# Optimization experiments

Measured on AMD Instinct MI355X. Metric: run time of the kernel, lower is better.

The kernel has to match this reference:

```python
import jax, jax.numpy as jnp
import numpy as np

DIM = 2048
N_HEADS = 16
HEAD_DIM = DIM // N_HEADS

def setup_inputs() -> dict:
    key = jax.random.key(0)
    kx, kqkv, kout = jax.random.split(key, 3)
    x = jax.random.normal(kx, (2, 2048, DIM), dtype=jnp.float32)
    # nn.Linear weights stored [out_features, in_features]; y = x @ W.T
    W_qkv = jax.random.normal(kqkv, (3 * DIM, DIM), dtype=jnp.float32) * (DIM ** -0.5)
    W_out = jax.random.normal(kout, (DIM, DIM), dtype=jnp.float32) * (DIM ** -0.5)
    return {"x": x, "W_qkv": W_qkv, "W_out": W_out}

def reference(x, W_qkv, W_out):
    B, T, D = x.shape
    qkv = jnp.einsum('btd,ed->bte', x, W_qkv)  # [B,T,3D]
    q, k, v = jnp.split(qkv, 3, axis=-1)
    def heads(t):
        return t.reshape(B, T, N_HEADS, HEAD_DIM).transpose(0, 2, 1, 3)  # [B,H,T,d]
    q, k, v = heads(q), heads(k), heads(v)
    att = jnp.einsum('bhid,bhjd->bhij', q, k) / (HEAD_DIM ** 0.5)
    causal = jnp.tril(jnp.ones((T, T), dtype=bool))
    att = jnp.where(causal, att, -jnp.inf)
    att = jax.nn.softmax(att, axis=-1)
    out = jnp.einsum('bhij,bhjd->bhid', att, v)
    out = out.transpose(0, 2, 1, 3).reshape(B, T, D)
    return jnp.einsum('btd,ed->bte', out, W_out)
```

## Files before the change

### kernel.cpp

```cpp
#include <hip/hip_runtime.h>

typedef short short8 __attribute__((ext_vector_type(8)));
typedef short short4v __attribute__((ext_vector_type(4)));
typedef float f32x4 __attribute__((ext_vector_type(4)));
typedef unsigned short u16;
typedef u16 ushort4v __attribute__((ext_vector_type(4)));

__device__ inline u16 f2bf(float f){
  unsigned int u = __builtin_bit_cast(unsigned int, f);
  u = (u + 0x7fffu + ((u >> 16) & 1u)) >> 16;
  return (u16)u;
}

__device__ inline short8 cat8(short4v a, short4v b){
  short8 r;
  r[0]=a[0]; r[1]=a[1]; r[2]=a[2]; r[3]=a[3];
  r[4]=b[0]; r[5]=b[1]; r[6]=b[2]; r[7]=b[3];
  return r;
}

__device__ inline void gload_lds16(const void* g, unsigned lds_addr){
  __builtin_amdgcn_global_load_lds((__attribute__((address_space(1))) void*)(uintptr_t)g,
                                   (__attribute__((address_space(3))) void*)(uintptr_t)lds_addr,
                                   16, 0, 0);
}

__global__ void cvt_bf16(const float* __restrict__ in, u16* __restrict__ out, int n4){
  int stride = gridDim.x * blockDim.x;
  for (int i = blockIdx.x * blockDim.x + threadIdx.x; i < n4; i += stride){
    float4 v = ((const float4*)in)[i];
    ushort4v r = { f2bf(v.x), f2bf(v.y), f2bf(v.z), f2bf(v.w) };
    ((ushort4v*)out)[i] = r;
  }
}

template<int OUT_BF16>
__global__ __launch_bounds__(256) void gemm_bt(const u16* __restrict__ A, const u16* __restrict__ B,
                                               void* __restrict__ Cv, int M, int N, int K){
  __shared__ u16 As[128 * 64];
  __shared__ u16 Bs[128 * 64];
  const int tid  = threadIdx.x;
  const int wave = tid >> 6, lane = tid & 63;
  const int lr = lane & 15, lg = lane >> 4;
  const int wm = wave >> 1, wn = wave & 1;

  const int bid = blockIdx.y * gridDim.x + blockIdx.x;
  const int cpx = (gridDim.x * gridDim.y) >> 3;
  const int swz = (bid & 7) * cpx + (bid >> 3);
  const long bm = (swz & 31) * 128L;
  const long bn = (swz >> 5) * 128L;

  const unsigned asb = (unsigned)(uintptr_t)As;
  const unsigned bsb = (unsigned)(uintptr_t)Bs;

  const int  srow = wave * 32 + (lane >> 3);
  const int  scol = ((lane & 7) ^ (lane >> 3)) * 8;
  const u16* aptr = A + (bm + srow) * (long)K + scol;
  const u16* bptr = B + (bn + srow) * (long)K + scol;
  const unsigned sdst = (unsigned)(wave * 4096);

  f32x4 acc[4][4] = {};
  for (int k0 = 0; k0 < K; k0 += 64){
    #pragma unroll
    for (int c = 0; c < 4; c++){
      gload_lds16(aptr + (size_t)(8 * c) * K + k0, asb + sdst + 1024u * c);
      gload_lds16(bptr + (size_t)(8 * c) * K + k0, bsb + sdst + 1024u * c);
    }
    __syncthreads();
    #pragma unroll
    for (int kk = 0; kk < 2; kk++){
      short8 af[4], bfr[4];
      #pragma unroll
      for (int m = 0; m < 4; m++){
        int row = wm * 64 + m * 16 + lr;
        int phys = (kk * 4 + lg) ^ (row & 7);
        af[m] = *(const short8*)&As[row * 64 + phys * 8];
      }
      #pragma unroll
      for (int n = 0; n < 4; n++){
        int row = wn * 64 + n * 16 + lr;
        int phys = (kk * 4 + lg) ^ (row & 7);
        bfr[n] = *(const short8*)&Bs[row * 64 + phys * 8];
      }
      #pragma unroll
      for (int m = 0; m < 4; m++)
        #pragma unroll
        for (int n = 0; n < 4; n++)
          acc[m][n] = __builtin_amdgcn_mfma_f32_16x16x32_bf16(af[m], bfr[n], acc[m][n], 0, 0, 0);
    }
    __syncthreads();
  }
  #pragma unroll
  for (int m = 0; m < 4; m++){
    #pragma unroll
    for (int n = 0; n < 4; n++){
      #pragma unroll
      for (int r = 0; r < 4; r++){
        long row = bm + wm*64 + m*16 + lg*4 + r;
        long col = bn + wn*64 + n*16 + lr;
        float v = acc[m][n][r];
        if (OUT_BF16) ((u16*)Cv)[row * (long)N + col] = f2bf(v);
        else          ((float*)Cv)[row * (long)N + col] = v;
      }
    }
  }
}

__global__ __launch_bounds__(256, 2) void attn_fwd(const u16* __restrict__ qkv, u16* __restrict__ out){
  const int T = 2048, D3 = 6144, D = 2048, HD = 128;
  const int bh = blockIdx.x;
  const int pr = blockIdx.y;
  const int b = bh >> 4, h = bh & 15;
  const int tid = threadIdx.x, wave = tid >> 6, lane = tid & 63;
  const int lr = lane & 15, lg = lane >> 4;

  __shared__ u16 Klds[64][136];
  __shared__ u16 Vlds[64][136];
  __shared__ u16 Plds[4][16][72];

  const size_t base = (size_t)b * T * D3;
  const unsigned vtr = (unsigned)(uintptr_t)&Vlds[(lane >> 4) * 8 + ((lane >> 2) & 3)][(lane & 3) * 4];

  const int srow = tid >> 4;
  const int scol = (tid & 15) * 8;
  const u16* kgp = qkv + base + (size_t)srow * D3 + D + h * HD + scol;
  const u16* vgp = kgp + D;

  for (int half = 0; half < 2; half++){
    const int qt = half ? pr : (31 - pr);
    const int q0 = qt * 64;
    const int q0w = q0 + wave * 16;

    short8 qf[4];
    {
      const u16* qrow = qkv + base + (size_t)(q0w + lr) * D3 + h * HD;
      #pragma unroll
      for (int kk = 0; kk < 4; kk++)
        qf[kk] = *(const short8*)(qrow + kk*32 + lg*8);
    }

    f32x4 o[8] = {};
    float mrow[4], lrw[4];
    #pragma unroll
    for (int r = 0; r < 4; r++){ mrow[r] = -1e30f; lrw[r] = 0.f; }

    const int ntiles = qt + 1;
    short8 kreg[4], vreg[4];
    #pragma unroll
    for (int c = 0; c < 4; c++){
      kreg[c] = *(const short8*)(kgp + (size_t)(16 * c) * D3);
      vreg[c] = *(const short8*)(vgp + (size_t)(16 * c) * D3);
    }

    for (int t = 0; t < ntiles; t++){
      const int k0 = t * 64;
      __syncthreads();
      #pragma unroll
      for (int c = 0; c < 4; c++){
        *(short8*)&Klds[srow + 16*c][scol] = kreg[c];
        *(short8*)&Vlds[srow + 16*c][scol] = vreg[c];
      }
      __syncthreads();
      if (t + 1 < ntiles){
        const u16* kn = kgp + (size_t)(k0 + 64) * D3;
        const u16* vn = vgp + (size_t)(k0 + 64) * D3;
        #pragma unroll
        for (int c = 0; c < 4; c++){
          kreg[c] = *(const short8*)(kn + (size_t)(16 * c) * D3);
          vreg[c] = *(const short8*)(vn + (size_t)(16 * c) * D3);
        }
      }

      f32x4 s[4] = {};
      #pragma unroll
      for (int kh = 0; kh < 4; kh++){
        #pragma unroll
        for (int kk = 0; kk < 4; kk++){
          short8 kfrag = *(const short8*)&Klds[kh*16 + lr][kk*32 + lg*8];
          s[kh] = __builtin_amdgcn_mfma_f32_16x16x32_bf16(qf[kk], kfrag, s[kh], 0, 0, 0);
        }
      }
      const float scale = 0.08838834764831845f;
      const bool need_mask = (k0 + 63 > q0w);
      #pragma unroll
      for (int kh = 0; kh < 4; kh++){
        int key = k0 + kh*16 + lr;
        #pragma unroll
        for (int r = 0; r < 4; r++){
          float v = s[kh][r] * scale;
          if (need_mask && key > q0w + lg*4 + r) v = -1e30f;
          s[kh][r] = v;
        }
      }
      float fs[4];
      #pragma unroll
      for (int r = 0; r < 4; r++){
        float mx = fmaxf(fmaxf(s[0][r], s[1][r]), fmaxf(s[2][r], s[3][r]));
        #pragma unroll
        for (int msk = 8; msk >= 1; msk >>= 1)
          mx = fmaxf(mx, __shfl_xor(mx, msk, 64));
        float mnew = fmaxf(mrow[r], mx);
        float f = __expf(mrow[r] - mnew);
        float p0 = __expf(s[0][r] - mnew);
        float p1 = __expf(s[1][r] - mnew);
        float p2 = __expf(s[2][r] - mnew);
        float p3 = __expf(s[3][r] - mnew);
        s[0][r] = p0; s[1][r] = p1; s[2][r] = p2; s[3][r] = p3;
        float rs = (p0 + p1) + (p2 + p3);
        #pragma unroll
        for (int msk = 8; msk >= 1; msk >>= 1)
          rs += __shfl_xor(rs, msk, 64);
        lrw[r] = lrw[r] * f + rs;
        mrow[r] = mnew;
        fs[r] = f;
      }
      #pragma unroll
      for (int dt = 0; dt < 8; dt++)
        #pragma unroll
        for (int r = 0; r < 4; r++)
          o[dt][r] *= fs[r];
      #pragma unroll
      for (int kh = 0; kh < 4; kh++)
        #pragma unroll
        for (int r = 0; r < 4; r++)
          Plds[wave][lg*4 + r][kh*16 + lr] = f2bf(s[kh][r]);
      asm volatile("s_waitcnt lgkmcnt(0)" ::: "memory");
      __builtin_amdgcn_sched_barrier(0);
      short8 pf[2];
      #pragma unroll
      for (int kp2 = 0; kp2 < 2; kp2++)
        pf[kp2] = *(const short8*)&Plds[wave][lr][kp2*32 + lg*8];
      asm volatile("s_waitcnt lgkmcnt(0)" ::: "memory");
      __builtin_amdgcn_sched_barrier(0);

      short4v vf[2][2][2];
      #define TR4(BUF, PTR) \
        asm volatile("ds_read_b64_tr_b16 %0, %1"             : "=v"(vf[BUF][0][0]) : "v"(PTR)); \
        asm volatile("ds_read_b64_tr_b16 %0, %1 offset:1088" : "=v"(vf[BUF][0][1]) : "v"(PTR)); \
        asm volatile("ds_read_b64_tr_b16 %0, %1 offset:8704" : "=v"(vf[BUF][1][0]) : "v"(PTR)); \
        asm volatile("ds_read_b64_tr_b16 %0, %1 offset:9792" : "=v"(vf[BUF][1][1]) : "v"(PTR));
      TR4(0, vtr)
      #pragma unroll
      for (int dt = 0; dt < 8; dt++){
        if (dt < 7){
          unsigned pn = vtr + (unsigned)((dt + 1) * 32);
          TR4((dt + 1) & 1, pn)
          asm volatile("s_waitcnt lgkmcnt(4)" ::: "memory");
        } else {
          asm volatile("s_waitcnt lgkmcnt(0)" ::: "memory");
        }
        __builtin_amdgcn_sched_barrier(0);
        short8 v0 = cat8(vf[dt & 1][0][0], vf[dt & 1][0][1]);
        short8 v1 = cat8(vf[dt & 1][1][0], vf[dt & 1][1][1]);
        o[dt] = __builtin_amdgcn_mfma_f32_16x16x32_bf16(pf[0], v0, o[dt], 0, 0, 0);
        o[dt] = __builtin_amdgcn_mfma_f32_16x16x32_bf16(pf[1], v1, o[dt], 0, 0, 0);
      }
      #undef TR4
    }
    float rl[4];
    #pragma unroll
    for (int r = 0; r < 4; r++) rl[r] = 1.0f / lrw[r];
    #pragma unroll
    for (int dt = 0; dt < 8; dt++){
      #pragma unroll
      for (int r = 0; r < 4; r++){
        float v = o[dt][r] * rl[r];
        int qa = q0w + lg*4 + r;
        out[(size_t)(b * T + qa) * D + h * HD + dt*16 + lr] = f2bf(v);
      }
    }
  }
}

extern "C" void kernel_launch(void* const* d_in, const int* in_sizes, int n_in,
                              void* d_out, int out_size, void* d_ws, size_t ws_size,
                              hipStream_t stream) {
  const float* x    = (const float*)d_in[0];
  const float* wqkv = (const float*)d_in[1];
  const float* wout = (const float*)d_in[2];
  float* out = (float*)d_out;

  u16* ws    = (u16*)d_ws;
  u16* xb    = ws;
  u16* wqkvb = xb + 8388608;
  u16* qkvb  = wqkvb + 12582912;
  u16* attnb = xb;
  u16* woutb = wqkvb;

  cvt_bf16<<<2048, 256, 0, stream>>>(x,    xb,    8388608 / 4);
  cvt_bf16<<<2048, 256, 0, stream>>>(wqkv, wqkvb, 12582912 / 4);

  gemm_bt<1><<<dim3(32, 48), 256, 0, stream>>>(xb, wqkvb, qkvb, 4096, 6144, 2048);

  cvt_bf16<<<2048, 256, 0, stream>>>(wout, woutb, 4194304 / 4);

  attn_fwd<<<dim3(32, 16), 256, 0, stream>>>(qkvb, attnb);

  gemm_bt<0><<<dim3(32, 16), 256, 0, stream>>>(attnb, woutb, out, 4096, 2048, 2048);
}
```

Baseline: 293.4 us.

## Share K/V tiles between paired query tiles and skip rescale lazily

The attention kernel now processes its two paired query tiles (high and low) at the same time. Each K/V tile is loaded into LDS once and used by both, where before the loads were repeated in two sequential passes. Softmax now works in base 2 with exp2f and a pre-scaled log2e factor. It also skips the max update and the output rescale when the new row max stays within a threshold of the running max. The GEMM block swizzle is removed and replaced with a plain blockIdx mapping. The costs are more registers for two accumulator sets, which could lower occupancy, and some L2 locality lost in the GEMMs.

```diff
diff --git a/kernel.cpp b/kernel.cpp
--- a/kernel.cpp
+++ b/kernel.cpp
@@ -43,13 +43,7 @@
   const int wave = tid >> 6, lane = tid & 63;
   const int lr = lane & 15, lg = lane >> 4;
   const int wm = wave >> 1, wn = wave & 1;
-
-  const int bid = blockIdx.y * gridDim.x + blockIdx.x;
-  const int cpx = (gridDim.x * gridDim.y) >> 3;
-  const int swz = (bid & 7) * cpx + (bid >> 3);
-  const long bm = (swz & 31) * 128L;
-  const long bn = (swz >> 5) * 128L;
-
+  const long bm = blockIdx.x * 128L, bn = blockIdx.y * 128L;
   const unsigned asb = (unsigned)(uintptr_t)As;
   const unsigned bsb = (unsigned)(uintptr_t)Bs;
 
@@ -109,7 +103,7 @@
 __global__ __launch_bounds__(256, 2) void attn_fwd(const u16* __restrict__ qkv, u16* __restrict__ out){
   const int T = 2048, D3 = 6144, D = 2048, HD = 128;
   const int bh = blockIdx.x;
-  const int pr = blockIdx.y;
+  const int p = blockIdx.y;
   const int b = bh >> 4, h = bh & 15;
   const int tid = threadIdx.x, wave = tid >> 6, lane = tid & 63;
   const int lr = lane & 15, lg = lane >> 4;
@@ -126,148 +120,179 @@
   const u16* kgp = qkv + base + (size_t)srow * D3 + D + h * HD + scol;
   const u16* vgp = kgp + D;
 
-  for (int half = 0; half < 2; half++){
-    const int qt = half ? pr : (31 - pr);
-    const int q0 = qt * 64;
-    const int q0w = q0 + wave * 16;
-
-    short8 qf[4];
-    {
-      const u16* qrow = qkv + base + (size_t)(q0w + lr) * D3 + h * HD;
-      #pragma unroll
-      for (int kk = 0; kk < 4; kk++)
-        qf[kk] = *(const short8*)(qrow + kk*32 + lg*8);
-    }
-
-    f32x4 o[8] = {};
-    float mrow[4], lrw[4];
-    #pragma unroll
-    for (int r = 0; r < 4; r++){ mrow[r] = -1e30f; lrw[r] = 0.f; }
-
-    const int ntiles = qt + 1;
-    short8 kreg[4], vreg[4];
+  const int H = 31 - p, L = p;
+  const int q0A = H * 64 + wave * 16;
+  const int q0B = L * 64 + wave * 16;
+
+  short8 qfA[4], qfB[4];
+  {
+    const u16* qa = qkv + base + (size_t)(q0A + lr) * D3 + h * HD;
+    const u16* qb = qkv + base + (size_t)(q0B + lr) * D3 + h * HD;
+    #pragma unroll
+    for (int kk = 0; kk < 4; kk++){
+      qfA[kk] = *(const short8*)(qa + kk*32 + lg*8);
+      qfB[kk] = *(const short8*)(qb + kk*32 + lg*8);
+    }
+  }
+
+  f32x4 oA[8] = {}, oB[8] = {};
+  float mA[4], lA[4], mB[4], lB[4];
+  #pragma unroll
+  for (int r = 0; r < 4; r++){ mA[r] = -1e30f; lA[r] = 0.f; mB[r] = -1e30f; lB[r] = 0.f; }
+
+  const float scale2 = 0.12751971252971732f;
+  const float THR = 11.5f;
+
+  #define PROCESS(QF, O, MR, LW, Q0W, K0) { \
+    f32x4 s[4] = {}; \
+    _Pragma("unroll") \
+    for (int kh = 0; kh < 4; kh++){ \
+      _Pragma("unroll") \
+      for (int kk = 0; kk < 4; kk++){ \
+        short8 kfrag = *(const short8*)&Klds[kh*16 + lr][kk*32 + lg*8]; \
+        s[kh] = __builtin_amdgcn_mfma_f32_16x16x32_bf16(QF[kk], kfrag, s[kh], 0, 0, 0); \
+      } \
+    } \
+    const bool need_mask = ((K0) + 63 > (Q0W)); \
+    _Pragma("unroll") \
+    for (int kh = 0; kh < 4; kh++){ \
+      int key = (K0) + kh*16 + lr; \
+      _Pragma("unroll") \
+      for (int r = 0; r < 4; r++){ \
+        float v = s[kh][r] * scale2; \
+        if (need_mask && key > (Q0W) + lg*4 + r) v = -1e30f; \
+        s[kh][r] = v; \
+      } \
+    } \
+    float mx[4]; \
+    _Pragma("unroll") \
+    for (int r = 0; r < 4; r++){ \
+      float m0 = fmaxf(fmaxf(s[0][r], s[1][r]), fmaxf(s[2][r], s[3][r])); \
+      _Pragma("unroll") \
+      for (int msk = 8; msk >= 1; msk >>= 1) m0 = fmaxf(m0, __shfl_xor(m0, msk, 64)); \
+      mx[r] = m0; \
+    } \
+    bool cnd = (mx[0] <= MR[0] + THR) && (mx[1] <= MR[1] + THR) && \
+               (mx[2] <= MR[2] + THR) && (mx[3] <= MR[3] + THR); \
+    if (__all(cnd)){ \
+      _Pragma("unroll") \
+      for (int r = 0; r < 4; r++){ \
+        float p0 = exp2f(s[0][r] - MR[r]); \
+        float p1 = exp2f(s[1][r] - MR[r]); \
+        float p2 = exp2f(s[2][r] - MR[r]); \
+        float p3 = exp2f(s[3][r] - MR[r]); \
+        s[0][r] = p0; s[1][r] = p1; s[2][r] = p2; s[3][r] = p3; \
+        float rs = (p0 + p1) + (p2 + p3); \
+        _Pragma("unroll") \
+        for (int msk = 8; msk >= 1; msk >>= 1) rs += __shfl_xor(rs, msk, 64); \
+        LW[r] += rs; \
+      } \
+    } else { \
+      float fs[4]; \
+      _Pragma("unroll") \
+      for (int r = 0; r < 4; r++){ \
+        float mnew = fmaxf(MR[r], mx[r]); \
+        float f = exp2f(MR[r] - mnew); \
+        float p0 = exp2f(s[0][r] - mnew); \
+        float p1 = exp2f(s[1][r] - mnew); \
+        float p2 = exp2f(s[2][r] - mnew); \
+        float p3 = exp2f(s[3][r] - mnew); \
+        s[0][r] = p0; s[1][r] = p1; s[2][r] = p2; s[3][r] = p3; \
+        float rs = (p0 + p1) + (p2 + p3); \
+        _Pragma("unroll") \
+        for (int msk = 8; msk >= 1; msk >>= 1) rs += __shfl_xor(rs, msk, 64); \
+        LW[r] = LW[r] * f + rs; \
+        MR[r] = mnew; \
+        fs[r] = f; \
+      } \
+      _Pragma("unroll") \
+      for (int dt = 0; dt < 8; dt++) \
+        _Pragma("unroll") \
+        for (int r = 0; r < 4; r++) O[dt][r] *= fs[r]; \
+    } \
+    _Pragma("unroll") \
+    for (int kh = 0; kh < 4; kh++) \
+      _Pragma("unroll") \
+      for (int r = 0; r < 4; r++) \
+        Plds[wave][lg*4 + r][kh*16 + lr] = f2bf(s[kh][r]); \
+    asm volatile("s_waitcnt lgkmcnt(0)" ::: "memory"); \
+    __builtin_amdgcn_sched_barrier(0); \
+    short8 pf[2]; \
+    _Pragma("unroll") \
+    for (int kp2 = 0; kp2 < 2; kp2++) \
+      pf[kp2] = *(const short8*)&Plds[wave][lr][kp2*32 + lg*8]; \
+    asm volatile("s_waitcnt lgkmcnt(0)" ::: "memory"); \
+    __builtin_amdgcn_sched_barrier(0); \
+    short4v vf[2][2][2]; \
+    asm volatile("ds_read_b64_tr_b16 %0, %1"             : "=v"(vf[0][0][0]) : "v"(vtr)); \
+    asm volatile("ds_read_b64_tr_b16 %0, %1 offset:1088" : "=v"(vf[0][0][1]) : "v"(vtr)); \
+    asm volatile("ds_read_b64_tr_b16 %0, %1 offset:8704" : "=v"(vf[0][1][0]) : "v"(vtr)); \
+    asm volatile("ds_read_b64_tr_b16 %0, %1 offset:9792" : "=v"(vf[0][1][1]) : "v"(vtr)); \
+    _Pragma("unroll") \
+    for (int dt = 0; dt < 8; dt++){ \
+      if (dt < 7){ \
+        unsigned pn = vtr + (unsigned)((dt + 1) * 32); \
+        int bnx = (dt + 1) & 1; \
+        asm volatile("ds_read_b64_tr_b16 %0, %1"             : "=v"(vf[bnx][0][0]) : "v"(pn)); \
+        asm volatile("ds_read_b64_tr_b16 %0, %1 offset:1088" : "=v"(vf[bnx][0][1]) : "v"(pn)); \
+        asm volatile("ds_read_b64_tr_b16 %0, %1 offset:8704" : "=v"(vf[bnx][1][0]) : "v"(pn)); \
+        asm volatile("ds_read_b64_tr_b16 %0, %1 offset:9792" : "=v"(vf[bnx][1][1]) : "v"(pn)); \
+        asm volatile("s_waitcnt lgkmcnt(4)" ::: "memory"); \
+      } else { \
+        asm volatile("s_waitcnt lgkmcnt(0)" ::: "memory"); \
+      } \
+      __builtin_amdgcn_sched_barrier(0); \
+      short8 v0 = cat8(vf[dt & 1][0][0], vf[dt & 1][0][1]); \
+      short8 v1 = cat8(vf[dt & 1][1][0], vf[dt & 1][1][1]); \
+      O[dt] = __builtin_amdgcn_mfma_f32_16x16x32_bf16(pf[0], v0, O[dt], 0, 0, 0); \
+      O[dt] = __builtin_amdgcn_mfma_f32_16x16x32_bf16(pf[1], v1, O[dt], 0, 0, 0); \
+    } \
+  }
+
+  const int ntiles = H + 1;
+  short8 kreg[4], vreg[4];
+  #pragma unroll
+  for (int c = 0; c < 4; c++){
+    kreg[c] = *(const short8*)(kgp + (size_t)(16 * c) * D3);
+    vreg[c] = *(const short8*)(vgp + (size_t)(16 * c) * D3);
+  }
+
+  for (int t = 0; t < ntiles; t++){
+    const int k0 = t * 64;
+    __syncthreads();
     #pragma unroll
     for (int c = 0; c < 4; c++){
-      kreg[c] = *(const short8*)(kgp + (size_t)(16 * c) * D3);
-      vreg[c] = *(const short8*)(vgp + (size_t)(16 * c) * D3);
-    }
-
-    for (int t = 0; t < ntiles; t++){
-      const int k0 = t * 64;
-      __syncthreads();
+      *(short8*)&Klds[srow + 16*c][scol] = kreg[c];
+      *(short8*)&Vlds[srow + 16*c][scol] = vreg[c];
+    }
+    __syncthreads();
+    if (t + 1 < ntiles){
+      const u16* kn = kgp + (size_t)(k0 + 64) * D3;
+      const u16* vn = vgp + (size_t)(k0 + 64) * D3;
       #pragma unroll
       for (int c = 0; c < 4; c++){
-        *(short8*)&Klds[srow + 16*c][scol] = kreg[c];
-        *(short8*)&Vlds[srow + 16*c][scol] = vreg[c];
+        kreg[c] = *(const short8*)(kn + (size_t)(16 * c) * D3);
+        vreg[c] = *(const short8*)(vn + (size_t)(16 * c) * D3);
       }
-      __syncthreads();
-      if (t + 1 < ntiles){
-        const u16* kn = kgp + (size_t)(k0 + 64) * D3;
-        const u16* vn = vgp + (size_t)(k0 + 64) * D3;
-        #pragma unroll
-        for (int c = 0; c < 4; c++){
-          kreg[c] = *(const short8*)(kn + (size_t)(16 * c) * D3);
-          vreg[c] = *(const short8*)(vn + (size_t)(16 * c) * D3);
-        }
-      }
-
-      f32x4 s[4] = {};
-      #pragma unroll
-      for (int kh = 0; kh < 4; kh++){
-        #pragma unroll
-        for (int kk = 0; kk < 4; kk++){
-          short8 kfrag = *(const short8*)&Klds[kh*16 + lr][kk*32 + lg*8];
-          s[kh] = __builtin_amdgcn_mfma_f32_16x16x32_bf16(qf[kk], kfrag, s[kh], 0, 0, 0);
-        }
-      }
-      const float scale = 0.08838834764831845f;
-      const bool need_mask = (k0 + 63 > q0w);
-      #pragma unroll
-      for (int kh = 0; kh < 4; kh++){
-        int key = k0 + kh*16 + lr;
-        #pragma unroll
-        for (int r = 0; r < 4; r++){
-          float v = s[kh][r] * scale;
-          if (need_mask && key > q0w + lg*4 + r) v = -1e30f;
-          s[kh][r] = v;
-        }
-      }
-      float fs[4];
-      #pragma unroll
-      for (int r = 0; r < 4; r++){
-        float mx = fmaxf(fmaxf(s[0][r], s[1][r]), fmaxf(s[2][r], s[3][r]));
-        #pragma unroll
-        for (int msk = 8; msk >= 1; msk >>= 1)
-          mx = fmaxf(mx, __shfl_xor(mx, msk, 64));
-        float mnew = fmaxf(mrow[r], mx);
-        float f = __expf(mrow[r] - mnew);
-        float p0 = __expf(s[0][r] - mnew);
-        float p1 = __expf(s[1][r] - mnew);
-        float p2 = __expf(s[2][r] - mnew);
-        float p3 = __expf(s[3][r] - mnew);
-        s[0][r] = p0; s[1][r] = p1; s[2][r] = p2; s[3][r] = p3;
-        float rs = (p0 + p1) + (p2 + p3);
-        #pragma unroll
-        for (int msk = 8; msk >= 1; msk >>= 1)
-          rs += __shfl_xor(rs, msk, 64);
-        lrw[r] = lrw[r] * f + rs;
-        mrow[r] = mnew;
-        fs[r] = f;
-      }
-      #pragma unroll
-      for (int dt = 0; dt < 8; dt++)
-        #pragma unroll
-        for (int r = 0; r < 4; r++)
-          o[dt][r] *= fs[r];
-      #pragma unroll
-      for (int kh = 0; kh < 4; kh++)
-        #pragma unroll
-        for (int r = 0; r < 4; r++)
-          Plds[wave][lg*4 + r][kh*16 + lr] = f2bf(s[kh][r]);
-      asm volatile("s_waitcnt lgkmcnt(0)" ::: "memory");
-      __builtin_amdgcn_sched_barrier(0);
-      short8 pf[2];
-      #pragma unroll
-      for (int kp2 = 0; kp2 < 2; kp2++)
-        pf[kp2] = *(const short8*)&Plds[wave][lr][kp2*32 + lg*8];
-      asm volatile("s_waitcnt lgkmcnt(0)" ::: "memory");
-      __builtin_amdgcn_sched_barrier(0);
-
-      short4v vf[2][2][2];
-      #define TR4(BUF, PTR) \
-        asm volatile("ds_read_b64_tr_b16 %0, %1"             : "=v"(vf[BUF][0][0]) : "v"(PTR)); \
-        asm volatile("ds_read_b64_tr_b16 %0, %1 offset:1088" : "=v"(vf[BUF][0][1]) : "v"(PTR)); \
-        asm volatile("ds_read_b64_tr_b16 %0, %1 offset:8704" : "=v"(vf[BUF][1][0]) : "v"(PTR)); \
-        asm volatile("ds_read_b64_tr_b16 %0, %1 offset:9792" : "=v"(vf[BUF][1][1]) : "v"(PTR));
-      TR4(0, vtr)
-      #pragma unroll
-      for (int dt = 0; dt < 8; dt++){
-        if (dt < 7){
-          unsigned pn = vtr + (unsigned)((dt + 1) * 32);
-          TR4((dt + 1) & 1, pn)
-          asm volatile("s_waitcnt lgkmcnt(4)" ::: "memory");
-        } else {
-          asm volatile("s_waitcnt lgkmcnt(0)" ::: "memory");
-        }
-        __builtin_amdgcn_sched_barrier(0);
-        short8 v0 = cat8(vf[dt & 1][0][0], vf[dt & 1][0][1]);
-        short8 v1 = cat8(vf[dt & 1][1][0], vf[dt & 1][1][1]);
-        o[dt] = __builtin_amdgcn_mfma_f32_16x16x32_bf16(pf[0], v0, o[dt], 0, 0, 0);
-        o[dt] = __builtin_amdgcn_mfma_f32_16x16x32_bf16(pf[1], v1, o[dt], 0, 0, 0);
-      }
-      #undef TR4
-    }
-    float rl[4];
-    #pragma unroll
-    for (int r = 0; r < 4; r++) rl[r] = 1.0f / lrw[r];
-    #pragma unroll
-    for (int dt = 0; dt < 8; dt++){
-      #pragma unroll
-      for (int r = 0; r < 4; r++){
-        float v = o[dt][r] * rl[r];
-        int qa = q0w + lg*4 + r;
-        out[(size_t)(b * T + qa) * D + h * HD + dt*16 + lr] = f2bf(v);
-      }
+    }
+
+    PROCESS(qfA, oA, mA, lA, q0A, k0)
+    if (t <= L){
+      PROCESS(qfB, oB, mB, lB, q0B, k0)
+    }
+  }
+  #undef PROCESS
+
+  #pragma unroll
+  for (int r = 0; r < 4; r++){ lA[r] = 1.0f / lA[r]; lB[r] = 1.0f / lB[r]; }
+  #pragma unroll
+  for (int dt = 0; dt < 8; dt++){
+    #pragma unroll
+    for (int r = 0; r < 4; r++){
+      int qa = q0A + lg*4 + r;
+      out[(size_t)(b * T + qa) * D + h * HD + dt*16 + lr] = f2bf(oA[dt][r] * lA[r]);
+      int qb = q0B + lg*4 + r;
+      out[(size_t)(b * T + qb) * D + h * HD + dt*16 + lr] = f2bf(oB[dt][r] * lB[r]);
     }
   }
 }
```

New measurement: 282.0 us. -3.9%, faster.
